# Kernel tuning notes

Measured on AMD Instinct MI355X. Metric: run time of the kernel, lower is better.

## Reference

```python
import jax, jax.numpy as jnp
import numpy as np


def _gatv2(xs, xd, src, dst, Ws, bs, Wd, bd, a):
    # DGL GATv2Conv, num_heads=1: e = a . leaky_relu(W_s x_u + W_d x_v), edge softmax per dst,
    # out[v] = sum_u alpha_uv * (W_s x_u)
    n_dst = xd.shape[0]
    el = xs @ Ws + bs                      # [Ns, D]
    er = xd @ Wd + bd                      # [Nd, D]
    e = jax.nn.leaky_relu(el[src] + er[dst], negative_slope=0.2)  # [E, D]
    s = e @ a                              # [E]
    m = jax.ops.segment_max(s, dst, num_segments=n_dst)
    w = jnp.exp(s - m[dst])
    z = jax.ops.segment_sum(w, dst, num_segments=n_dst)
    alpha = w / z[dst]
    return jax.ops.segment_sum(alpha[:, None] * el[src], dst, num_segments=n_dst)


def _cheb_prop(x, src, dst, norm):
    # D^{-1/2} A D^{-1/2} x via gather/segment-sum (DGL ChebConv message passing)
    return jax.ops.segment_sum((x * norm)[src], dst, num_segments=x.shape[0]) * norm


def _forward(user_table, item_table,
             g1r_Ws, g1r_bs, g1r_Wd, g1r_bd, g1r_a,
             g1d_Ws, g1d_bs, g1d_Wd, g1d_bd, g1d_a,
             g2d_Ws, g2d_bs, g2d_Wd, g2d_bd, g2d_a,
             g2f_Ws, g2f_bs, g2f_Wd, g2f_bd, g2f_a,
             spec_Ws, spec_bs, spec_Wd, spec_bd, spec_a,
             cheb_W, cheb_b, out_W, out_b,
             mc_W, mc_b, ms_W, ms_b, pp_W, pp_b, ps_W, ps_b,
             lambda_max, rate_src, rate_dst, friend_src, friend_dst):
    u, it = user_table, item_table
    # spatial attention (heterogeneous GATv2 pipeline); 'rated' = reverse of 'rate'
    h1_item = _gatv2(u, it, rate_src, rate_dst, g1r_Ws, g1r_bs, g1r_Wd, g1r_bd, g1r_a)
    h2_user = _gatv2(it, u, rate_dst, rate_src, g1d_Ws, g1d_bs, g1d_Wd, g1d_bd, g1d_a)
    item_inf = _gatv2(h1_item, u, rate_dst, rate_src, g2d_Ws, g2d_bs, g2d_Wd, g2d_bd, g2d_a)
    social_it = _gatv2(h2_user, u, friend_src, friend_dst, g2f_Ws, g2f_bs, g2f_Wd, g2f_bd, g2f_a)
    user_pref = jnp.concatenate([item_inf, social_it], 1) @ out_W + out_b
    # spectral attention: ChebConv (k=3) on social graph, then GATv2
    deg = jax.ops.segment_sum(jnp.ones(friend_dst.shape, u.dtype), friend_dst,
                              num_segments=u.shape[0])
    norm = (jnp.maximum(deg, 1.0) ** -0.5)[:, None]
    re = 2.0 / lambda_max[0]
    X0 = u
    X1 = -re * _cheb_prop(X0, friend_src, friend_dst, norm) + X0 * (re - 1.0)
    X2 = (-2.0 * re * _cheb_prop(X1, friend_src, friend_dst, norm)
          + 2.0 * (re - 1.0) * X1 - X0)
    ch = jnp.concatenate([X0, X1, X2], 1) @ cheb_W + cheb_b
    user_social = _gatv2(ch, ch, friend_src, friend_dst,
                         spec_Ws, spec_bs, spec_Wd, spec_bd, spec_a)
    # mutualistic layer
    h_uP = jnp.concatenate([user_pref, u], 1) @ mc_W + mc_b
    h_uS = jnp.concatenate([user_social, u], 1) @ ms_W + ms_b
    h_m = h_uP * h_uS
    h_mP = h_m * jax.nn.softmax(h_uP, axis=1)
    h_mS = h_m * jax.nn.softmax(h_uS, axis=1)
    # prediction layer
    h_new_P = jnp.concatenate([h_mP, h_uP], 1) @ pp_W + pp_b
    h_new_S = jnp.concatenate([h_mS, h_uS], 1) @ ps_W + ps_b
    r_hat = h_new_P @ it.T   # [N_u, N_i]
    s_hat = h_new_S @ u.T    # [N_u, N_u]
    return r_hat, s_hat


def setup_inputs() -> dict:
    N_U, N_I, D, E_R, E_F = 8192, 8192, 64, 524288, 262144
    key = jax.random.key(0)
    ks = iter(jax.random.split(key, 64))

    def p(*shape):
        return jax.random.normal(next(ks), shape, dtype=jnp.float32) * 0.1

    inp = {"user_table": p(N_U, D), "item_table": p(N_I, D)}
    for nm in ["g1r", "g1d", "g2d", "g2f", "spec"]:
        inp[nm + "_Ws"] = p(D, D)
        inp[nm + "_bs"] = p(D)
        inp[nm + "_Wd"] = p(D, D)
        inp[nm + "_bd"] = p(D)
        inp[nm + "_a"] = p(D)
    inp["cheb_W"] = p(3 * D, D); inp["cheb_b"] = p(D)
    inp["out_W"] = p(2 * D, D); inp["out_b"] = p(D)
    inp["mc_W"] = p(2 * D, D); inp["mc_b"] = p(D)
    inp["ms_W"] = p(2 * D, D); inp["ms_b"] = p(D)
    inp["pp_W"] = p(2 * D, D); inp["pp_b"] = p(D)
    inp["ps_W"] = p(2 * D, D); inp["ps_b"] = p(D)
    inp["lambda_max"] = jnp.array([2.0], jnp.float32)
    inp["rate_src"] = jax.random.randint(next(ks), (E_R,), 0, N_U, dtype=jnp.int32)
    inp["rate_dst"] = jax.random.randint(next(ks), (E_R,), 0, N_I, dtype=jnp.int32)
    inp["friend_src"] = jax.random.randint(next(ks), (E_F,), 0, N_U, dtype=jnp.int32)
    inp["friend_dst"] = jax.random.randint(next(ks), (E_F,), 0, N_U, dtype=jnp.int32)
    return inp


def reference(user_table, item_table,
              g1r_Ws, g1r_bs, g1r_Wd, g1r_bd, g1r_a,
              g1d_Ws, g1d_bs, g1d_Wd, g1d_bd, g1d_a,
              g2d_Ws, g2d_bs, g2d_Wd, g2d_bd, g2d_a,
              g2f_Ws, g2f_bs, g2f_Wd, g2f_bd, g2f_a,
              spec_Ws, spec_bs, spec_Wd, spec_bd, spec_a,
              cheb_W, cheb_b, out_W, out_b,
              mc_W, mc_b, ms_W, ms_b, pp_W, pp_b, ps_W, ps_b,
              lambda_max, rate_src, rate_dst, friend_src, friend_dst):
    return _forward(user_table, item_table,
                    g1r_Ws, g1r_bs, g1r_Wd, g1r_bd, g1r_a,
                    g1d_Ws, g1d_bs, g1d_Wd, g1d_bd, g1d_a,
                    g2d_Ws, g2d_bs, g2d_Wd, g2d_bd, g2d_a,
                    g2f_Ws, g2f_bs, g2f_Wd, g2f_bd, g2f_a,
                    spec_Ws, spec_bs, spec_Wd, spec_bd, spec_a,
                    cheb_W, cheb_b, out_W, out_b,
                    mc_W, mc_b, ms_W, ms_b, pp_W, pp_b, ps_W, ps_b,
                    lambda_max, rate_src, rate_dst, friend_src, friend_dst)
```

## Files before the change

### kernel.cpp

```cpp
#include <hip/hip_runtime.h>
#include <math.h>

#define D 64

typedef float f32x4 __attribute__((ext_vector_type(4)));
typedef short short8 __attribute__((ext_vector_type(8)));

#define DPP_ADD(v, ctrl) \
  v += __builtin_bit_cast(float, __builtin_amdgcn_update_dpp(0, __builtin_bit_cast(int, v), ctrl, 0xF, 0xF, true))
#define DPP_MAX(v, ctrl) \
  v = fmaxf(v, __builtin_bit_cast(float, __builtin_amdgcn_update_dpp(0, __builtin_bit_cast(int, v), ctrl, 0xF, 0xF, true)))

__device__ __forceinline__ float red16_sum(float x) {
  DPP_ADD(x, 0xB1); DPP_ADD(x, 0x4E); DPP_ADD(x, 0x141); DPP_ADD(x, 0x140);
  return x;
}
__device__ __forceinline__ float wave_sum64(float x) {
  x = red16_sum(x);
  x += __shfl_xor(x, 16, 64);
  x += __shfl_xor(x, 32, 64);
  return x;
}
__device__ __forceinline__ float wave_max64(float x) {
  DPP_MAX(x, 0xB1); DPP_MAX(x, 0x4E); DPP_MAX(x, 0x141); DPP_MAX(x, 0x140);
  x = fmaxf(x, __shfl_xor(x, 16, 64));
  x = fmaxf(x, __shfl_xor(x, 32, 64));
  return x;
}

__device__ __forceinline__ float lrelu02(float x) { return (x > 0.f) ? x : 0.2f * x; }

__device__ __forceinline__ unsigned short f2bf_rne(float x) {
  unsigned int u = __builtin_bit_cast(unsigned int, x);
  unsigned int r = u + 0x7FFFu + ((u >> 16) & 1u);
  return (unsigned short)(r >> 16);
}
__device__ __forceinline__ float bf2f(unsigned short h) {
  unsigned int u = ((unsigned int)h) << 16;
  return __builtin_bit_cast(float, u);
}
__device__ __forceinline__ float deg_nrm(int d) {
  return rsqrtf(fmaxf((float)d, 1.0f));
}

__device__ __forceinline__ f32x4 gat_row4(const float* __restrict__ el,
                                          f32x4 er4, f32x4 a4,
                                          const int* __restrict__ col,
                                          int beg, int end, int g, int off) {
  f32x4 acc = {0.f, 0.f, 0.f, 0.f};
  float z = 0.f;
  for (int i = beg; i < end; i += 8) {
    bool act0 = (i + g) < end;
    bool act1 = (i + 4 + g) < end;
    int u0 = act0 ? col[i + g] : col[beg];
    int u1 = act1 ? col[i + 4 + g] : col[beg];
    f32x4 e0 = *reinterpret_cast<const f32x4*>(el + (size_t)u0 * D + off);
    f32x4 e1 = *reinterpret_cast<const f32x4*>(el + (size_t)u1 * D + off);
    float p0 = a4.x * lrelu02(e0.x + er4.x);
    p0 = fmaf(a4.y, lrelu02(e0.y + er4.y), p0);
    p0 = fmaf(a4.z, lrelu02(e0.z + er4.z), p0);
    p0 = fmaf(a4.w, lrelu02(e0.w + er4.w), p0);
    float p1 = a4.x * lrelu02(e1.x + er4.x);
    p1 = fmaf(a4.y, lrelu02(e1.y + er4.y), p1);
    p1 = fmaf(a4.z, lrelu02(e1.z + er4.z), p1);
    p1 = fmaf(a4.w, lrelu02(e1.w + er4.w), p1);
    p0 = red16_sum(p0);
    p1 = red16_sum(p1);
    float w0 = act0 ? __expf(p0) : 0.f;
    float w1 = act1 ? __expf(p1) : 0.f;
    z += w0 + w1;
    acc.x = fmaf(w0, e0.x, acc.x); acc.x = fmaf(w1, e1.x, acc.x);
    acc.y = fmaf(w0, e0.y, acc.y); acc.y = fmaf(w1, e1.y, acc.y);
    acc.z = fmaf(w0, e0.z, acc.z); acc.z = fmaf(w1, e1.z, acc.z);
    acc.w = fmaf(w0, e0.w, acc.w); acc.w = fmaf(w1, e1.w, acc.w);
  }
  acc.x += __shfl_xor(acc.x, 16, 64); acc.x += __shfl_xor(acc.x, 32, 64);
  acc.y += __shfl_xor(acc.y, 16, 64); acc.y += __shfl_xor(acc.y, 32, 64);
  acc.z += __shfl_xor(acc.z, 16, 64); acc.z += __shfl_xor(acc.z, 32, 64);
  acc.w += __shfl_xor(acc.w, 16, 64); acc.w += __shfl_xor(acc.w, 32, 64);
  z += __shfl_xor(z, 16, 64); z += __shfl_xor(z, 32, 64);
  f32x4 res;
  if (end > beg) {
    res.x = acc.x / z; res.y = acc.y / z; res.z = acc.z / z; res.w = acc.w / z;
  } else {
    res = f32x4{0.f, 0.f, 0.f, 0.f};
  }
  return res;
}

__device__ __forceinline__ void gemm4(const float* A0, const float* A1, const float* A2,
                                      int nparts, const float* W, const float* bias,
                                      int r0, int lane,
                                      float& acc0, float& acc1, float& acc2, float& acc3) {
  float bv = bias[lane];
  acc0 = bv; acc1 = bv; acc2 = bv; acc3 = bv;
  for (int p = 0; p < nparts; ++p) {
    const float* Ap = ((p == 0) ? A0 : (p == 1) ? A1 : A2) + (size_t)r0 * D;
    const float* Wp = W + p * D * D;
#pragma unroll 8
    for (int k = 0; k < D; ++k) {
      float wv = Wp[k * D + lane];
      acc0 = fmaf(Ap[k],         wv, acc0);
      acc1 = fmaf(Ap[k + D],     wv, acc1);
      acc2 = fmaf(Ap[k + 2 * D], wv, acc2);
      acc3 = fmaf(Ap[k + 3 * D], wv, acc3);
    }
  }
}

__device__ __forceinline__ void gemm_store(const float* A0, const float* A1, const float* A2,
                                           int nparts, const float* W, const float* bias,
                                           float* out, int bx, int w, int lane) {
  int r0 = __builtin_amdgcn_readfirstlane(bx * 16 + w * 4);
  float a0, a1, a2, a3;
  gemm4(A0, A1, A2, nparts, W, bias, r0, lane, a0, a1, a2, a3);
  out[(size_t)r0 * D + lane]       = a0;
  out[(size_t)(r0 + 1) * D + lane] = a1;
  out[(size_t)(r0 + 2) * D + lane] = a2;
  out[(size_t)(r0 + 3) * D + lane] = a3;
}

__device__ __forceinline__ void gat_task(const float* el, const float* er, const float* a,
                                         const int* cnt, const int* col, int cap,
                                         float* out, int N,
                                         int bx, int w, int lane, int g, int off) {
  int v = __builtin_amdgcn_readfirstlane(bx * 4 + w);
  if (v < N) {
    int dv = cnt[v];
    if (dv > cap) dv = cap;
    int beg = v * cap, end = beg + dv;
    f32x4 er4 = *reinterpret_cast<const f32x4*>(er + (size_t)v * D + off);
    f32x4 a4  = *reinterpret_cast<const f32x4*>(a + off);
    f32x4 res = gat_row4(el, er4, a4, col, beg, end, g, off);
    if (g == 0) *reinterpret_cast<f32x4*>(out + (size_t)v * D + off) = res;
  }
}

__device__ __forceinline__ void cheb_task(const float* xin, const float* xprev,
                                          const int* cnt, const float* lam,
                                          const int* col, int cap,
                                          float* out, int N, int mode,
                                          int bx, int w, int lane, int g, int off) {
  int v = __builtin_amdgcn_readfirstlane(bx * 4 + w);
  if (v >= N) return;
  float re = 2.0f / lam[0];
  int dv = cnt[v];
  if (dv > cap) dv = cap;
  int beg = v * cap, end = beg + dv;
  f32x4 acc = {0.f, 0.f, 0.f, 0.f};
  for (int i = beg; i < end; i += 8) {
    bool act0 = (i + g) < end;
    bool act1 = (i + 4 + g) < end;
    int u0 = act0 ? col[i + g] : col[beg];
    int u1 = act1 ? col[i + 4 + g] : col[beg];
    float n0 = act0 ? deg_nrm(cnt[u0]) : 0.f;
    float n1 = act1 ? deg_nrm(cnt[u1]) : 0.f;
    f32x4 e0 = *reinterpret_cast<const f32x4*>(xin + (size_t)u0 * D + off);
    f32x4 e1 = *reinterpret_cast<const f32x4*>(xin + (size_t)u1 * D + off);
    acc.x = fmaf(n0, e0.x, acc.x); acc.x = fmaf(n1, e1.x, acc.x);
    acc.y = fmaf(n0, e0.y, acc.y); acc.y = fmaf(n1, e1.y, acc.y);
    acc.z = fmaf(n0, e0.z, acc.z); acc.z = fmaf(n1, e1.z, acc.z);
    acc.w = fmaf(n0, e0.w, acc.w); acc.w = fmaf(n1, e1.w, acc.w);
  }
  acc.x += __shfl_xor(acc.x, 16, 64); acc.x += __shfl_xor(acc.x, 32, 64);
  acc.y += __shfl_xor(acc.y, 16, 64); acc.y += __shfl_xor(acc.y, 32, 64);
  acc.z += __shfl_xor(acc.z, 16, 64); acc.z += __shfl_xor(acc.z, 32, 64);
  acc.w += __shfl_xor(acc.w, 16, 64); acc.w += __shfl_xor(acc.w, 32, 64);
  if (g == 0) {
    float nv = deg_nrm(cnt[v]);
    f32x4 xi = *reinterpret_cast<const f32x4*>(xin + (size_t)v * D + off);
    f32x4 o;
    if (mode == 1) {
      o.x = -re * (acc.x * nv) + xi.x * (re - 1.0f);
      o.y = -re * (acc.y * nv) + xi.y * (re - 1.0f);
      o.z = -re * (acc.z * nv) + xi.z * (re - 1.0f);
      o.w = -re * (acc.w * nv) + xi.w * (re - 1.0f);
    } else {
      f32x4 xp = *reinterpret_cast<const f32x4*>(xprev + (size_t)v * D + off);
      o.x = -2.0f * re * (acc.x * nv) + 2.0f * (re - 1.0f) * xi.x - xp.x;
      o.y = -2.0f * re * (acc.y * nv) + 2.0f * (re - 1.0f) * xi.y - xp.y;
      o.z = -2.0f * re * (acc.z * nv) + 2.0f * (re - 1.0f) * xi.z - xp.z;
      o.w = -2.0f * re * (acc.w * nv) + 2.0f * (re - 1.0f) * xi.w - xp.w;
    }
    *reinterpret_cast<f32x4*>(out + (size_t)v * D + off) = o;
  }
}

__device__ __forceinline__ void split_task(const float* src, unsigned short* outh,
                                           size_t NFl, int bx, int tid) {
  size_t i = ((size_t)bx * 256 + tid) * 4;
  if (i < NFl) {
    float4 xv = *reinterpret_cast<const float4*>(src + i);
    ushort4 hv, lv;
    hv.x = f2bf_rne(xv.x); lv.x = f2bf_rne(xv.x - bf2f(hv.x));
    hv.y = f2bf_rne(xv.y); lv.y = f2bf_rne(xv.y - bf2f(hv.y));
    hv.z = f2bf_rne(xv.z); lv.z = f2bf_rne(xv.z - bf2f(hv.z));
    hv.w = f2bf_rne(xv.w); lv.w = f2bf_rne(xv.w - bf2f(hv.w));
    *reinterpret_cast<ushort4*>(outh + i) = hv;
    *reinterpret_cast<ushort4*>(outh + NFl + i) = lv;
  }
}

#define K_GEMM  0
#define K_GEMM2 1
#define K_GAT   2
#define K_CHEB  3
#define K_SPLIT 4

struct Slice {
  const float *a0, *a1, *a2;
  const float *w, *b;
  const float *w2, *b2;
  const int *cnt, *col;
  float *out;
  unsigned short *outh;
  int kind, nparts, N, nblk, mode, cap;
};
struct Pack { Slice s[10]; };

__global__ void __launch_bounds__(256) mega_k(Pack pk, int nsl) {
  __shared__ float lds[16][D];
  int si = 0, rem = blockIdx.x;
#pragma unroll
  for (int c = 0; c < 9; ++c) {
    int nb = pk.s[c].nblk;
    if (si == c && c < nsl - 1 && rem >= nb) { rem -= nb; si = c + 1; }
  }
  int bx = rem;
  Slice S;
  if      (si == 0) S = pk.s[0];
  else if (si == 1) S = pk.s[1];
  else if (si == 2) S = pk.s[2];
  else if (si == 3) S = pk.s[3];
  else if (si == 4) S = pk.s[4];
  else if (si == 5) S = pk.s[5];
  else if (si == 6) S = pk.s[6];
  else if (si == 7) S = pk.s[7];
  else if (si == 8) S = pk.s[8];
  else              S = pk.s[9];

  int w = threadIdx.x >> 6, lane = threadIdx.x & 63;
  int g = lane >> 4, off = (lane & 15) << 2;

  if (S.kind == K_GEMM) {
    gemm_store(S.a0, S.a1, S.a2, S.nparts, S.w, S.b, S.out, bx, w, lane);
  } else if (S.kind == K_GEMM2) {
    int r0 = __builtin_amdgcn_readfirstlane(bx * 16 + w * 4);
    float t0, t1, t2, t3;
    gemm4(S.a0, S.a1, nullptr, S.nparts, S.w, S.b, r0, lane, t0, t1, t2, t3);
    lds[w * 4 + 0][lane] = t0;
    lds[w * 4 + 1][lane] = t1;
    lds[w * 4 + 2][lane] = t2;
    lds[w * 4 + 3][lane] = t3;
    __syncthreads();
    float bv = S.b2[lane];
    float c0 = bv, c1 = bv, c2 = bv, c3 = bv;
    const float* Xp = S.a2 + (size_t)r0 * D;
#pragma unroll 8
    for (int k = 0; k < D; ++k) {
      float wv = S.w2[k * D + lane];
      c0 = fmaf(lds[w * 4 + 0][k], wv, c0);
      c1 = fmaf(lds[w * 4 + 1][k], wv, c1);
      c2 = fmaf(lds[w * 4 + 2][k], wv, c2);
      c3 = fmaf(lds[w * 4 + 3][k], wv, c3);
    }
#pragma unroll 8
    for (int k = 0; k < D; ++k) {
      float wv = S.w2[(D + k) * D + lane];
      c0 = fmaf(Xp[k],         wv, c0);
      c1 = fmaf(Xp[k + D],     wv, c1);
      c2 = fmaf(Xp[k + 2 * D], wv, c2);
      c3 = fmaf(Xp[k + 3 * D], wv, c3);
    }
    S.out[(size_t)r0 * D + lane]       = c0;
    S.out[(size_t)(r0 + 1) * D + lane] = c1;
    S.out[(size_t)(r0 + 2) * D + lane] = c2;
    S.out[(size_t)(r0 + 3) * D + lane] = c3;
  } else if (S.kind == K_GAT) {
    gat_task(S.a0, S.a1, S.w, S.cnt, S.col, S.cap, S.out, S.N, bx, w, lane, g, off);
  } else if (S.kind == K_CHEB) {
    cheb_task(S.a0, S.a1, S.cnt, S.b, S.col, S.cap, S.out, S.N, S.mode, bx, w, lane, g, off);
  } else {
    split_task(S.a0, S.outh, (size_t)S.N, bx, threadIdx.x);
  }
}

__global__ void __launch_bounds__(256) scat3_k(
    const int* __restrict__ rate_src, const int* __restrict__ rate_dst,
    const int* __restrict__ friend_src, const int* __restrict__ friend_dst,
    int ER, int EF, int capR, int capF,
    int* __restrict__ cnt_Rd, int* __restrict__ cnt_Rs, int* __restrict__ cnt_Fd,
    int* __restrict__ col_Rd, int* __restrict__ col_Rs, int* __restrict__ col_Fd) {
  int i = blockIdx.x * blockDim.x + threadIdx.x;
  if (i < ER) {
    int d = rate_dst[i];
    int pos = atomicAdd(&cnt_Rd[d], 1);
    if (pos < capR) col_Rd[(size_t)d * capR + pos] = rate_src[i];
  } else if (i < 2 * ER) {
    int j = i - ER;
    int s = rate_src[j];
    int pos = atomicAdd(&cnt_Rs[s], 1);
    if (pos < capR) col_Rs[(size_t)s * capR + pos] = rate_dst[j];
  } else if (i < 2 * ER + EF) {
    int j = i - 2 * ER;
    int d = friend_dst[j];
    int pos = atomicAdd(&cnt_Fd[d], 1);
    if (pos < capF) col_Fd[(size_t)d * capF + pos] = friend_src[j];
  }
}

__global__ void __launch_bounds__(256) tail_k(
    const float* __restrict__ el, const float* __restrict__ er, const float* __restrict__ a,
    const int* __restrict__ cnt, const int* __restrict__ col, int cap,
    const float* __restrict__ u, const float* __restrict__ huP,
    const float* __restrict__ msW, const float* __restrict__ msb,
    const float* __restrict__ ppW, const float* __restrict__ ppb,
    const float* __restrict__ psW, const float* __restrict__ psb,
    unsigned short* __restrict__ Phl, unsigned short* __restrict__ Shl, int N) {
  __shared__ float l_us[8][D];
  __shared__ float l_mP[8][D];
  __shared__ float l_mS[8][D];
  __shared__ float l_uP[8][D];
  __shared__ float l_uS[8][D];
  const size_t NF = (size_t)N * D;
  int w = threadIdx.x >> 6, lane = threadIdx.x & 63;
  int g = lane >> 4, off = (lane & 15) << 2;
  int v0 = blockIdx.x * 8;
  f32x4 a4 = *reinterpret_cast<const f32x4*>(a + off);
#pragma unroll
  for (int j = 0; j < 2; ++j) {
    int r = w * 2 + j;
    int v = __builtin_amdgcn_readfirstlane(v0 + r);
    int dv = cnt[v];
    if (dv > cap) dv = cap;
    int beg = v * cap, end = beg + dv;
    f32x4 er4 = *reinterpret_cast<const f32x4*>(er + (size_t)v * D + off);
    f32x4 res = gat_row4(el, er4, a4, col, beg, end, g, off);
    if (g == 0) *reinterpret_cast<f32x4*>(&l_us[r][off]) = res;
  }
  __syncthreads();
#pragma unroll
  for (int j = 0; j < 2; ++j) {
    int r = w * 2 + j;
    int v = __builtin_amdgcn_readfirstlane(v0 + r);
    const float* ur = u + (size_t)v * D;
    float acc = msb[lane];
#pragma unroll 8
    for (int k = 0; k < D; ++k) acc = fmaf(l_us[r][k], msW[k * D + lane], acc);
#pragma unroll 8
    for (int k = 0; k < D; ++k) acc = fmaf(ur[k], msW[(D + k) * D + lane], acc);
    float hS = acc;
    float hP = huP[(size_t)v * D + lane];
    float hm = hP * hS;
    float ep = __expf(hP - wave_max64(hP));
    float es = __expf(hS - wave_max64(hS));
    float mP = hm * ep / wave_sum64(ep);
    float mS = hm * es / wave_sum64(es);
    l_uP[r][lane] = hP; l_uS[r][lane] = hS;
    l_mP[r][lane] = mP; l_mS[r][lane] = mS;
  }
  __syncthreads();
#pragma unroll
  for (int j = 0; j < 2; ++j) {
    int r = w * 2 + j;
    size_t v = (size_t)(v0 + r);
    float aP = ppb[lane], aS = psb[lane];
#pragma unroll 8
    for (int k = 0; k < D; ++k) {
      aP = fmaf(l_mP[r][k], ppW[k * D + lane], aP);
      aS = fmaf(l_mS[r][k], psW[k * D + lane], aS);
    }
#pragma unroll 8
    for (int k = 0; k < D; ++k) {
      aP = fmaf(l_uP[r][k], ppW[(D + k) * D + lane], aP);
      aS = fmaf(l_uS[r][k], psW[(D + k) * D + lane], aS);
    }
    unsigned short h = f2bf_rne(aP);
    Phl[v * D + lane] = h;
    Phl[NF + v * D + lane] = f2bf_rne(aP - bf2f(h));
    h = f2bf_rne(aS);
    Shl[v * D + lane] = h;
    Shl[NF + v * D + lane] = f2bf_rne(aS - bf2f(h));
  }
}

__device__ __forceinline__ void mfma_tile(const unsigned short* Ah, const unsigned short* Bh,
                                          float* Cp, int ldc, size_t NF,
                                          int row0, int col0, int lane) {
  const unsigned short* Al = Ah + NF;
  const unsigned short* Bl = Bh + NF;
  int r = lane & 15, q = lane >> 4;
  short8 ah00, ah01, ah10, ah11, al00, al01, al10, al11;
  {
    size_t r0 = (size_t)(row0 + r) * D;
    size_t r1 = (size_t)(row0 + 16 + r) * D;
    int ko = q * 8;
    ah00 = *reinterpret_cast<const short8*>(Ah + r0 + ko);
    ah01 = *reinterpret_cast<const short8*>(Ah + r0 + 32 + ko);
    ah10 = *reinterpret_cast<const short8*>(Ah + r1 + ko);
    ah11 = *reinterpret_cast<const short8*>(Ah + r1 + 32 + ko);
    al00 = *reinterpret_cast<const short8*>(Al + r0 + ko);
    al01 = *reinterpret_cast<const short8*>(Al + r0 + 32 + ko);
    al10 = *reinterpret_cast<const short8*>(Al + r1 + ko);
    al11 = *reinterpret_cast<const short8*>(Al + r1 + 32 + ko);
  }
  for (int jt = 0; jt < 8; ++jt) {
    size_t brow = (size_t)(col0 + jt * 16 + r) * D;
    int ko = q * 8;
    short8 bh0 = *reinterpret_cast<const short8*>(Bh + brow + ko);
    short8 bh1 = *reinterpret_cast<const short8*>(Bh + brow + 32 + ko);
    short8 bl0 = *reinterpret_cast<const short8*>(Bl + brow + ko);
    short8 bl1 = *reinterpret_cast<const short8*>(Bl + brow + 32 + ko);

    f32x4 acc0 = {0.f, 0.f, 0.f, 0.f};
    f32x4 acc1 = {0.f, 0.f, 0.f, 0.f};
    acc0 = __builtin_amdgcn_mfma_f32_16x16x32_bf16(bh0, ah00, acc0, 0, 0, 0);
    acc0 = __builtin_amdgcn_mfma_f32_16x16x32_bf16(bl0, ah00, acc0, 0, 0, 0);
    acc0 = __builtin_amdgcn_mfma_f32_16x16x32_bf16(bh0, al00, acc0, 0, 0, 0);
    acc0 = __builtin_amdgcn_mfma_f32_16x16x32_bf16(bh1, ah01, acc0, 0, 0, 0);
    acc0 = __builtin_amdgcn_mfma_f32_16x16x32_bf16(bl1, ah01, acc0, 0, 0, 0);
    acc0 = __builtin_amdgcn_mfma_f32_16x16x32_bf16(bh1, al01, acc0, 0, 0, 0);
    acc1 = __builtin_amdgcn_mfma_f32_16x16x32_bf16(bh0, ah10, acc1, 0, 0, 0);
    acc1 = __builtin_amdgcn_mfma_f32_16x16x32_bf16(bl0, ah10, acc1, 0, 0, 0);
    acc1 = __builtin_amdgcn_mfma_f32_16x16x32_bf16(bh0, al10, acc1, 0, 0, 0);
    acc1 = __builtin_amdgcn_mfma_f32_16x16x32_bf16(bh1, ah11, acc1, 0, 0, 0);
    acc1 = __builtin_amdgcn_mfma_f32_16x16x32_bf16(bl1, ah11, acc1, 0, 0, 0);
    acc1 = __builtin_amdgcn_mfma_f32_16x16x32_bf16(bh1, al11, acc1, 0, 0, 0);

    *reinterpret_cast<f32x4*>(&Cp[(size_t)(row0 + r) * ldc + col0 + jt * 16 + q * 4])      = acc0;
    *reinterpret_cast<f32x4*>(&Cp[(size_t)(row0 + 16 + r) * ldc + col0 + jt * 16 + q * 4]) = acc1;
  }
}

__global__ void __launch_bounds__(256) mfma_abt_k(
    const unsigned short* __restrict__ Phi, const unsigned short* __restrict__ Ihi,
    const unsigned short* __restrict__ Shi, const unsigned short* __restrict__ Uhi,
    float* __restrict__ outP, float* __restrict__ outS, int ldc, size_t NF) {
  const unsigned short *Ah, *Bh;
  float* Cp;
  if (blockIdx.z == 0) { Ah = Phi; Bh = Ihi; Cp = outP; }
  else                 { Ah = Shi; Bh = Uhi; Cp = outS; }
  int nwg = gridDim.x * gridDim.y;
  int lin = blockIdx.y * gridDim.x + blockIdx.x;
  int cpx = nwg >> 3;
  int swz = (lin & 7) * cpx + (lin >> 3);
  int bxx = swz % gridDim.x;
  int byy = swz / gridDim.x;
  int w = threadIdx.x >> 6, lane = threadIdx.x & 63;
  mfma_tile(Ah, Bh, Cp, ldc, NF, byy * 128 + w * 32, bxx * 128, lane);
}

static void slice_gemm(Slice& s, const float* A0, const float* A1, const float* A2,
                       int nparts, const float* W, const float* b, float* out, int N) {
  s.kind = K_GEMM; s.a0 = A0; s.a1 = A1; s.a2 = A2; s.nparts = nparts;
  s.w = W; s.b = b; s.out = out; s.N = N; s.nblk = N / 16;
}
static void slice_gat(Slice& s, const float* el, const float* er, const float* a,
                      const int* cnt, const int* col, int cap, float* out, int N) {
  s.kind = K_GAT; s.a0 = el; s.a1 = er; s.w = a; s.cnt = cnt; s.col = col; s.cap = cap;
  s.out = out; s.N = N; s.nblk = N / 4;
}
static void slice_cheb(Slice& s, const float* xin, const float* xprev, const int* cnt,
                       const float* lam, const int* col, int cap, float* out, int N, int mode) {
  s.kind = K_CHEB; s.a0 = xin; s.a1 = xprev; s.cnt = cnt; s.b = lam; s.col = col; s.cap = cap;
  s.out = out; s.N = N; s.nblk = N / 4; s.mode = mode;
}
static void slice_split(Slice& s, const float* src, unsigned short* outh, int nelem) {
  s.kind = K_SPLIT; s.a0 = src; s.outh = outh; s.N = nelem; s.nblk = nelem / 1024;
}
static int pack_blocks(const Pack& p, int n) {
  int t = 0;
  for (int i = 0; i < n; ++i) t += p.s[i].nblk;
  return t;
}

extern "C" void kernel_launch(void* const* d_in, const int* in_sizes, int n_in,
                              void* d_out, int out_size, void* d_ws, size_t ws_size,
                              hipStream_t stream) {
  (void)n_in; (void)out_size; (void)ws_size;
  const float* u  = (const float*)d_in[0];
  const float* it = (const float*)d_in[1];
  const float* g1r_Ws = (const float*)d_in[2];  const float* g1r_bs = (const float*)d_in[3];
  const float* g1r_Wd = (const float*)d_in[4];  const float* g1r_bd = (const float*)d_in[5];
  const float* g1r_a  = (const float*)d_in[6];
  const float* g1d_Ws = (const float*)d_in[7];  const float* g1d_bs = (const float*)d_in[8];
  const float* g1d_Wd = (const float*)d_in[9];  const float* g1d_bd = (const float*)d_in[10];
  const float* g1d_a  = (const float*)d_in[11];
  const float* g2d_Ws = (const float*)d_in[12]; const float* g2d_bs = (const float*)d_in[13];
  const float* g2d_Wd = (const float*)d_in[14]; const float* g2d_bd = (const float*)d_in[15];
  const float* g2d_a  = (const float*)d_in[16];
  const float* g2f_Ws = (const float*)d_in[17]; const float* g2f_bs = (const float*)d_in[18];
  const float* g2f_Wd = (const float*)d_in[19]; const float* g2f_bd = (const float*)d_in[20];
  const float* g2f_a  = (const float*)d_in[21];
  const float* spec_Ws = (const float*)d_in[22]; const float* spec_bs = (const float*)d_in[23];
  const float* spec_Wd = (const float*)d_in[24]; const float* spec_bd = (const float*)d_in[25];
  const float* spec_a  = (const float*)d_in[26];
  const float* cheb_W = (const float*)d_in[27]; const float* cheb_b = (const float*)d_in[28];
  const float* out_W  = (const float*)d_in[29]; const float* out_b  = (const float*)d_in[30];
  const float* mc_W   = (const float*)d_in[31]; const float* mc_b   = (const float*)d_in[32];
  const float* ms_W   = (const float*)d_in[33]; const float* ms_b   = (const float*)d_in[34];
  const float* pp_W   = (const float*)d_in[35]; const float* pp_b   = (const float*)d_in[36];
  const float* ps_W   = (const float*)d_in[37]; const float* ps_b   = (const float*)d_in[38];
  const float* lambda_max = (const float*)d_in[39];
  const int* rate_src   = (const int*)d_in[40];
  const int* rate_dst   = (const int*)d_in[41];
  const int* friend_src = (const int*)d_in[42];
  const int* friend_dst = (const int*)d_in[43];

  const int NU = in_sizes[0] / D;
  const int NI = in_sizes[1] / D;
  const int ER = in_sizes[40];
  const int EF = in_sizes[42];
  const size_t NF = (size_t)NU * D;
  const int CAPR = 256;
  const int CAPF = 128;

  float* p = (float*)d_ws;
  float* E1 = p; p += NF;  float* R1 = p; p += NF;
  float* E2 = p; p += NF;  float* R2 = p; p += NF;
  float* E3 = p; p += NF;  float* R3 = p; p += NF;
  float* E4 = p; p += NF;  float* R4 = p; p += NF;
  float* E5 = p; p += NF;  float* R5 = p; p += NF;
  float* X1 = p; p += NF;  float* X2 = p; p += NF;
  float* H1 = p; p += NF;  float* H2 = p; p += NF;
  float* CH = p; p += NF;  float* IINF = p; p += NF;
  float* SOC = p; p += NF; float* HUP = p; p += NF;
  unsigned short* Uhl = (unsigned short*)p; p += NF;
  unsigned short* Ihl = (unsigned short*)p; p += NF;
  unsigned short* Phl = (unsigned short*)p; p += NF;
  unsigned short* Shl = (unsigned short*)p; p += NF;
  int* ip = (int*)p;
  int* cnt_Rd = ip;  ip += NI;
  int* cnt_Rs = ip;  ip += NU;
  int* cnt_Fd = ip;  ip += NU;
  int* col_Rd = ip;  ip += (size_t)NI * CAPR;
  int* col_Rs = ip;  ip += (size_t)NU * CAPR;
  int* col_Fd = ip;  ip += (size_t)NU * CAPF;

  dim3 b256(256);
  float* outf = (float*)d_out;

  hipMemsetAsync(cnt_Rd, 0, (size_t)(NI + NU + NU) * sizeof(int), stream);

  int totE = 2 * ER + EF;
  scat3_k<<<(totE + 255) / 256, b256, 0, stream>>>(rate_src, rate_dst, friend_src, friend_dst,
                                                   ER, EF, CAPR, CAPF,
                                                   cnt_Rd, cnt_Rs, cnt_Fd,
                                                   col_Rd, col_Rs, col_Fd);

  {
    Pack pk = {};
    slice_gemm(pk.s[0], u,  nullptr, nullptr, 1, g1r_Ws, g1r_bs, E1, NU);
    slice_gemm(pk.s[1], it, nullptr, nullptr, 1, g1r_Wd, g1r_bd, R1, NI);
    slice_gemm(pk.s[2], it, nullptr, nullptr, 1, g1d_Ws, g1d_bs, E2, NI);
    slice_gemm(pk.s[3], u,  nullptr, nullptr, 1, g1d_Wd, g1d_bd, R2, NU);
    slice_split(pk.s[4], u,  Uhl, (int)NF);
    slice_split(pk.s[5], it, Ihl, (int)NF);
    mega_k<<<pack_blocks(pk, 6), b256, 0, stream>>>(pk, 6);
  }
  {
    Pack pk = {};
    slice_gat(pk.s[0], E1, R1, g1r_a, cnt_Rd, col_Rd, CAPR, H1, NI);
    slice_gat(pk.s[1], E2, R2, g1d_a, cnt_Rs, col_Rs, CAPR, H2, NU);
    slice_cheb(pk.s[2], u, nullptr, cnt_Fd, lambda_max, col_Fd, CAPF, X1, NU, 1);
    mega_k<<<pack_blocks(pk, 3), b256, 0, stream>>>(pk, 3);
  }
  {
    Pack pk = {};
    slice_gemm(pk.s[0], H1, nullptr, nullptr, 1, g2d_Ws, g2d_bs, E3, NI);
    slice_gemm(pk.s[1], u,  nullptr, nullptr, 1, g2d_Wd, g2d_bd, R3, NU);
    slice_gemm(pk.s[2], H2, nullptr, nullptr, 1, g2f_Ws, g2f_bs, E4, NU);
    slice_gemm(pk.s[3], u,  nullptr, nullptr, 1, g2f_Wd, g2f_bd, R4, NU);
    slice_cheb(pk.s[4], X1, u, cnt_Fd, lambda_max, col_Fd, CAPF, X2, NU, 2);
    mega_k<<<pack_blocks(pk, 5), b256, 0, stream>>>(pk, 5);
  }
  {
    Pack pk = {};
    slice_gat(pk.s[0], E3, R3, g2d_a, cnt_Rs, col_Rs, CAPR, IINF, NU);
    slice_gat(pk.s[1], E4, R4, g2f_a, cnt_Fd, col_Fd, CAPF, SOC, NU);
    slice_gemm(pk.s[2], u, X1, X2, 3, cheb_W, cheb_b, CH, NU);
    mega_k<<<pack_blocks(pk, 3), b256, 0, stream>>>(pk, 3);
  }
  {
    Pack pk = {};
    pk.s[0].kind = K_GEMM2;
    pk.s[0].a0 = IINF; pk.s[0].a1 = SOC; pk.s[0].nparts = 2;
    pk.s[0].w = out_W; pk.s[0].b = out_b;
    pk.s[0].a2 = u; pk.s[0].w2 = mc_W; pk.s[0].b2 = mc_b;
    pk.s[0].out = HUP; pk.s[0].N = NU; pk.s[0].nblk = NU / 16;
    slice_gemm(pk.s[1], CH, nullptr, nullptr, 1, spec_Ws, spec_bs, E5, NU);
    slice_gemm(pk.s[2], CH, nullptr, nullptr, 1, spec_Wd, spec_bd, R5, NU);
    mega_k<<<pack_blocks(pk, 3), b256, 0, stream>>>(pk, 3);
  }
  tail_k<<<NU / 8, b256, 0, stream>>>(E5, R5, spec_a, cnt_Fd, col_Fd, CAPF, u, HUP,
                                      ms_W, ms_b, pp_W, pp_b, ps_W, ps_b, Phl, Shl, NU);
  mfma_abt_k<<<dim3(NI / 128, NU / 128, 2), b256, 0, stream>>>(
      Phl, Ihl, Shl, Uhl, outf, outf + (size_t)NU * NI, NI, NF);
}
```

Measured before the change: 464.3 us.

## Fuse edge scatter into first mega kernel and unroll gather loops by four

Drops the separate scatter kernel and runs the three CSR-bucketing passes as slices of the first packed mega kernel, alongside the projection GEMMs and bf16 splits, which saves one launch and its serialization gap. The GAT and Chebyshev gather loops get an unpredicated main loop that handles 16 neighbours per iteration, so more gathers are in flight at once, with the old loop kept for the tail. The MFMA GEMM output stores become nontemporal. The risk is higher register pressure in the unrolled loops and changed cache behaviour for GEMM outputs that later kernels read.

```diff
diff --git a/kernel.cpp b/kernel.cpp
--- a/kernel.cpp
+++ b/kernel.cpp
@@ -49,7 +49,44 @@
                                           int beg, int end, int g, int off) {
   f32x4 acc = {0.f, 0.f, 0.f, 0.f};
   float z = 0.f;
-  for (int i = beg; i < end; i += 8) {
+  int i = beg;
+  for (; i + 16 <= end; i += 16) {
+    int u0 = col[i + g];
+    int u1 = col[i + 4 + g];
+    int u2 = col[i + 8 + g];
+    int u3 = col[i + 12 + g];
+    f32x4 e0 = *reinterpret_cast<const f32x4*>(el + (size_t)u0 * D + off);
+    f32x4 e1 = *reinterpret_cast<const f32x4*>(el + (size_t)u1 * D + off);
+    f32x4 e2 = *reinterpret_cast<const f32x4*>(el + (size_t)u2 * D + off);
+    f32x4 e3 = *reinterpret_cast<const f32x4*>(el + (size_t)u3 * D + off);
+    float p0 = a4.x * lrelu02(e0.x + er4.x);
+    p0 = fmaf(a4.y, lrelu02(e0.y + er4.y), p0);
+    p0 = fmaf(a4.z, lrelu02(e0.z + er4.z), p0);
+    p0 = fmaf(a4.w, lrelu02(e0.w + er4.w), p0);
+    float p1 = a4.x * lrelu02(e1.x + er4.x);
+    p1 = fmaf(a4.y, lrelu02(e1.y + er4.y), p1);
+    p1 = fmaf(a4.z, lrelu02(e1.z + er4.z), p1);
+    p1 = fmaf(a4.w, lrelu02(e1.w + er4.w), p1);
+    float p2 = a4.x * lrelu02(e2.x + er4.x);
+    p2 = fmaf(a4.y, lrelu02(e2.y + er4.y), p2);
+    p2 = fmaf(a4.z, lrelu02(e2.z + er4.z), p2);
+    p2 = fmaf(a4.w, lrelu02(e2.w + er4.w), p2);
+    float p3 = a4.x * lrelu02(e3.x + er4.x);
+    p3 = fmaf(a4.y, lrelu02(e3.y + er4.y), p3);
+    p3 = fmaf(a4.z, lrelu02(e3.z + er4.z), p3);
+    p3 = fmaf(a4.w, lrelu02(e3.w + er4.w), p3);
+    p0 = red16_sum(p0);
+    p1 = red16_sum(p1);
+    p2 = red16_sum(p2);
+    p3 = red16_sum(p3);
+    float w0 = __expf(p0), w1 = __expf(p1), w2 = __expf(p2), w3 = __expf(p3);
+    z += (w0 + w1) + (w2 + w3);
+    acc.x = fmaf(w0, e0.x, fmaf(w1, e1.x, fmaf(w2, e2.x, fmaf(w3, e3.x, acc.x))));
+    acc.y = fmaf(w0, e0.y, fmaf(w1, e1.y, fmaf(w2, e2.y, fmaf(w3, e3.y, acc.y))));
+    acc.z = fmaf(w0, e0.z, fmaf(w1, e1.z, fmaf(w2, e2.z, fmaf(w3, e3.z, acc.z))));
+    acc.w = fmaf(w0, e0.w, fmaf(w1, e1.w, fmaf(w2, e2.w, fmaf(w3, e3.w, acc.w))));
+  }
+  for (; i < end; i += 8) {
     bool act0 = (i + g) < end;
     bool act1 = (i + 4 + g) < end;
     int u0 = act0 ? col[i + g] : col[beg];
@@ -148,7 +185,26 @@
   if (dv > cap) dv = cap;
   int beg = v * cap, end = beg + dv;
   f32x4 acc = {0.f, 0.f, 0.f, 0.f};
-  for (int i = beg; i < end; i += 8) {
+  int i = beg;
+  for (; i + 16 <= end; i += 16) {
+    int u0 = col[i + g];
+    int u1 = col[i + 4 + g];
+    int u2 = col[i + 8 + g];
+    int u3 = col[i + 12 + g];
+    float n0 = deg_nrm(cnt[u0]);
+    float n1 = deg_nrm(cnt[u1]);
+    float n2 = deg_nrm(cnt[u2]);
+    float n3 = deg_nrm(cnt[u3]);
+    f32x4 e0 = *reinterpret_cast<const f32x4*>(xin + (size_t)u0 * D + off);
+    f32x4 e1 = *reinterpret_cast<const f32x4*>(xin + (size_t)u1 * D + off);
+    f32x4 e2 = *reinterpret_cast<const f32x4*>(xin + (size_t)u2 * D + off);
+    f32x4 e3 = *reinterpret_cast<const f32x4*>(xin + (size_t)u3 * D + off);
+    acc.x = fmaf(n0, e0.x, fmaf(n1, e1.x, fmaf(n2, e2.x, fmaf(n3, e3.x, acc.x))));
+    acc.y = fmaf(n0, e0.y, fmaf(n1, e1.y, fmaf(n2, e2.y, fmaf(n3, e3.y, acc.y))));
+    acc.z = fmaf(n0, e0.z, fmaf(n1, e1.z, fmaf(n2, e2.z, fmaf(n3, e3.z, acc.z))));
+    acc.w = fmaf(n0, e0.w, fmaf(n1, e1.w, fmaf(n2, e2.w, fmaf(n3, e3.w, acc.w))));
+  }
+  for (; i < end; i += 8) {
     bool act0 = (i + g) < end;
     bool act1 = (i + 4 + g) < end;
     int u0 = act0 ? col[i + g] : col[beg];
@@ -206,12 +262,14 @@
 #define K_GAT   2
 #define K_CHEB  3
 #define K_SPLIT 4
+#define K_SCAT  5
 
 struct Slice {
   const float *a0, *a1, *a2;
   const float *w, *b;
   const float *w2, *b2;
-  const int *cnt, *col;
+  int *cnt;
+  const int *col;
   float *out;
   unsigned short *outh;
   int kind, nparts, N, nblk, mode, cap;
@@ -280,32 +338,17 @@
     gat_task(S.a0, S.a1, S.w, S.cnt, S.col, S.cap, S.out, S.N, bx, w, lane, g, off);
   } else if (S.kind == K_CHEB) {
     cheb_task(S.a0, S.a1, S.cnt, S.b, S.col, S.cap, S.out, S.N, S.mode, bx, w, lane, g, off);
+  } else if (S.kind == K_SPLIT) {
+    split_task(S.a0, S.outh, (size_t)S.N, bx, threadIdx.x);
   } else {
-    split_task(S.a0, S.outh, (size_t)S.N, bx, threadIdx.x);
-  }
-}
-
-__global__ void __launch_bounds__(256) scat3_k(
-    const int* __restrict__ rate_src, const int* __restrict__ rate_dst,
-    const int* __restrict__ friend_src, const int* __restrict__ friend_dst,
-    int ER, int EF, int capR, int capF,
-    int* __restrict__ cnt_Rd, int* __restrict__ cnt_Rs, int* __restrict__ cnt_Fd,
-    int* __restrict__ col_Rd, int* __restrict__ col_Rs, int* __restrict__ col_Fd) {
-  int i = blockIdx.x * blockDim.x + threadIdx.x;
-  if (i < ER) {
-    int d = rate_dst[i];
-    int pos = atomicAdd(&cnt_Rd[d], 1);
-    if (pos < capR) col_Rd[(size_t)d * capR + pos] = rate_src[i];
-  } else if (i < 2 * ER) {
-    int j = i - ER;
-    int s = rate_src[j];
-    int pos = atomicAdd(&cnt_Rs[s], 1);
-    if (pos < capR) col_Rs[(size_t)s * capR + pos] = rate_dst[j];
-  } else if (i < 2 * ER + EF) {
-    int j = i - 2 * ER;
-    int d = friend_dst[j];
-    int pos = atomicAdd(&cnt_Fd[d], 1);
-    if (pos < capF) col_Fd[(size_t)d * capF + pos] = friend_src[j];
+    int i = bx * 256 + threadIdx.x;
+    if (i < S.N) {
+      int d = S.col[i];
+      int pos = atomicAdd(S.cnt + d, 1);
+      if (pos < S.cap)
+        reinterpret_cast<int*>(S.out)[(size_t)d * S.cap + pos] =
+            reinterpret_cast<const int*>(S.a0)[i];
+    }
   }
 }
 
@@ -427,8 +470,10 @@
     acc1 = __builtin_amdgcn_mfma_f32_16x16x32_bf16(bl1, ah11, acc1, 0, 0, 0);
     acc1 = __builtin_amdgcn_mfma_f32_16x16x32_bf16(bh1, al11, acc1, 0, 0, 0);
 
-    *reinterpret_cast<f32x4*>(&Cp[(size_t)(row0 + r) * ldc + col0 + jt * 16 + q * 4])      = acc0;
-    *reinterpret_cast<f32x4*>(&Cp[(size_t)(row0 + 16 + r) * ldc + col0 + jt * 16 + q * 4]) = acc1;
+    __builtin_nontemporal_store(acc0,
+        reinterpret_cast<f32x4*>(&Cp[(size_t)(row0 + r) * ldc + col0 + jt * 16 + q * 4]));
+    __builtin_nontemporal_store(acc1,
+        reinterpret_cast<f32x4*>(&Cp[(size_t)(row0 + 16 + r) * ldc + col0 + jt * 16 + q * 4]));
   }
 }
 
@@ -456,17 +501,22 @@
   s.w = W; s.b = b; s.out = out; s.N = N; s.nblk = N / 16;
 }
 static void slice_gat(Slice& s, const float* el, const float* er, const float* a,
-                      const int* cnt, const int* col, int cap, float* out, int N) {
+                      int* cnt, const int* col, int cap, float* out, int N) {
   s.kind = K_GAT; s.a0 = el; s.a1 = er; s.w = a; s.cnt = cnt; s.col = col; s.cap = cap;
   s.out = out; s.N = N; s.nblk = N / 4;
 }
-static void slice_cheb(Slice& s, const float* xin, const float* xprev, const int* cnt,
+static void slice_cheb(Slice& s, const float* xin, const float* xprev, int* cnt,
                        const float* lam, const int* col, int cap, float* out, int N, int mode) {
   s.kind = K_CHEB; s.a0 = xin; s.a1 = xprev; s.cnt = cnt; s.b = lam; s.col = col; s.cap = cap;
   s.out = out; s.N = N; s.nblk = N / 4; s.mode = mode;
 }
 static void slice_split(Slice& s, const float* src, unsigned short* outh, int nelem) {
   s.kind = K_SPLIT; s.a0 = src; s.outh = outh; s.N = nelem; s.nblk = nelem / 1024;
+}
+static void slice_scat(Slice& s, const int* dst, const int* src, int* cnt, int* colout,
+                       int cap, int E) {
+  s.kind = K_SCAT; s.col = dst; s.a0 = (const float*)src; s.cnt = cnt;
+  s.out = (float*)colout; s.cap = cap; s.N = E; s.nblk = (E + 255) / 256;
 }
 static int pack_blocks(const Pack& p, int n) {
   int t = 0;
@@ -542,21 +592,18 @@
 
   hipMemsetAsync(cnt_Rd, 0, (size_t)(NI + NU + NU) * sizeof(int), stream);
 
-  int totE = 2 * ER + EF;
-  scat3_k<<<(totE + 255) / 256, b256, 0, stream>>>(rate_src, rate_dst, friend_src, friend_dst,
-                                                   ER, EF, CAPR, CAPF,
-                                                   cnt_Rd, cnt_Rs, cnt_Fd,
-                                                   col_Rd, col_Rs, col_Fd);
-
   {
     Pack pk = {};
-    slice_gemm(pk.s[0], u,  nullptr, nullptr, 1, g1r_Ws, g1r_bs, E1, NU);
-    slice_gemm(pk.s[1], it, nullptr, nullptr, 1, g1r_Wd, g1r_bd, R1, NI);
-    slice_gemm(pk.s[2], it, nullptr, nullptr, 1, g1d_Ws, g1d_bs, E2, NI);
-    slice_gemm(pk.s[3], u,  nullptr, nullptr, 1, g1d_Wd, g1d_bd, R2, NU);
-    slice_split(pk.s[4], u,  Uhl, (int)NF);
-    slice_split(pk.s[5], it, Ihl, (int)NF);
-    mega_k<<<pack_blocks(pk, 6), b256, 0, stream>>>(pk, 6);
+    slice_scat(pk.s[0], rate_dst, rate_src, cnt_Rd, col_Rd, CAPR, ER);
+    slice_scat(pk.s[1], rate_src, rate_dst, cnt_Rs, col_Rs, CAPR, ER);
+    slice_scat(pk.s[2], friend_dst, friend_src, cnt_Fd, col_Fd, CAPF, EF);
+    slice_gemm(pk.s[3], u,  nullptr, nullptr, 1, g1r_Ws, g1r_bs, E1, NU);
+    slice_gemm(pk.s[4], it, nullptr, nullptr, 1, g1r_Wd, g1r_bd, R1, NI);
+    slice_gemm(pk.s[5], it, nullptr, nullptr, 1, g1d_Ws, g1d_bs, E2, NI);
+    slice_gemm(pk.s[6], u,  nullptr, nullptr, 1, g1d_Wd, g1d_bd, R2, NU);
+    slice_split(pk.s[7], u,  Uhl, (int)NF);
+    slice_split(pk.s[8], it, Ihl, (int)NF);
+    mega_k<<<pack_blocks(pk, 9), b256, 0, stream>>>(pk, 9);
   }
   {
     Pack pk = {};
```

Result: faster. 406.8 us (-12.4%).
